# Performance work log

Measured on AMD Instinct MI355X. Metric: run time of the kernel, lower is better.

Reference implementation:

```python
import jax, jax.numpy as jnp
import numpy as np

N = 50000
E = 300000
D_IN = 128
H = 256
D_OUT = 256


def _glorot(key, shape):
    fan_in, fan_out = shape[0], shape[1]
    lim = float(np.sqrt(6.0 / (fan_in + fan_out)))
    return jax.random.uniform(key, shape, jnp.float32, -lim, lim)


def setup_inputs() -> dict:
    key = jax.random.key(0)
    ks = jax.random.split(key, 12)
    x = jax.random.normal(ks[0], (N, D_IN), jnp.float32)
    edge_index = jax.random.randint(ks[1], (2, E), 0, N, jnp.int64)
    return {
        "x": x,
        "edge_index": edge_index,
        "W1": _glorot(ks[2], (D_IN, H)),  "b1": jnp.zeros((H,), jnp.float32),
        "Wg1": _glorot(ks[3], (H, H)),    "bg1": jnp.zeros((H,), jnp.float32),
        "Wg2": _glorot(ks[4], (H, H)),    "bg2": jnp.zeros((H,), jnp.float32),
        "W2": _glorot(ks[5], (H, H)),     "b2": jnp.zeros((H,), jnp.float32),
        "W3": _glorot(ks[6], (H, D_OUT)), "b3": jnp.zeros((D_OUT,), jnp.float32),
    }


def _gcn_conv(h, src, dst, W, b):
    # PyG GCNConv: h' = D^-1/2 (A + I) D^-1/2 (h W) + b, deg counted at target with self-loops
    h = h @ W                                           # [N, H]
    deg = jnp.zeros((N,), h.dtype).at[dst].add(1.0) + 1.0
    dinv = jax.lax.rsqrt(deg)                           # deg^-1/2, [N]
    norm = dinv[src] * dinv[dst]                        # [E]
    msg = h[src] * norm[:, None]                        # gather + scale, [E, H]
    agg = jax.ops.segment_sum(msg, dst, num_segments=N)  # scatter-add
    agg = agg + h * (dinv * dinv)[:, None]              # self-loop contribution (norm = 1/deg)
    return agg + b


def reference(x, edge_index, W1, b1, Wg1, bg1, Wg2, bg2, W2, b2, W3, b3):
    src, dst = edge_index[0], edge_index[1]
    h = jax.nn.relu(x @ W1 + b1)
    h = jax.nn.relu(_gcn_conv(h, src, dst, Wg1, bg1))
    h = jax.nn.relu(_gcn_conv(h, src, dst, Wg2, bg2))
    h = jax.nn.relu(h @ W2 + b2)
    return jax.nn.softmax(h @ W3 + b3, axis=1)
```

## Files before the change

kernel.cpp:

```cpp
#include <hip/hip_runtime.h>
#include <math.h>

#define HDIM 256

typedef float floatx4 __attribute__((ext_vector_type(4)));
typedef __bf16 bf16x8 __attribute__((ext_vector_type(8)));
typedef unsigned short ushortx4 __attribute__((ext_vector_type(4)));
typedef unsigned short ushortx8 __attribute__((ext_vector_type(8)));

#define AS1C(p) ((const __attribute__((address_space(1))) void*)(p))
#define AS3(p)  ((__attribute__((address_space(3))) void*)(p))

__device__ inline unsigned short bf16_rn(float f) {
  unsigned u = __float_as_uint(f);
  return (unsigned short)((u + 0x7FFFu + ((u >> 16) & 1u)) >> 16);
}

__device__ inline void split_f32(float f, unsigned short& h, unsigned short& l) {
  unsigned short hb = bf16_rn(f);
  float hf = __uint_as_float(((unsigned)hb) << 16);
  h = hb;
  l = bf16_rn(f - hf);
}


__global__ __launch_bounds__(256)
void prep_w_staged(const float* __restrict__ W, unsigned short* __restrict__ SH,
                   unsigned short* __restrict__ SL, int K) {
  int idx = blockIdx.x * 256 + threadIdx.x;
  int total = K * 32;
  if (idx >= total) return;
  int chunksPerCb = total >> 1;
  int cb = (idx >= chunksPerCb) ? 1 : 0;
  int rem = idx - cb * chunksPerCb;
  int kt = rem >> 9;
  int chunk = rem & 511;
  int kc = chunk >> 7;
  int col = chunk & 127;
  const float* src = W + (size_t)(kt * 32 + kc * 8) * HDIM + cb * 128 + col;
#pragma unroll
  for (int e = 0; e < 8; ++e) {
    unsigned short h, l;
    split_f32(src[(size_t)e * HDIM], h, l);
    SH[(size_t)idx * 8 + e] = h;
    SL[(size_t)idx * 8 + e] = l;
  }
}


__global__ __launch_bounds__(256)
void split_plane(const float* __restrict__ in, unsigned short* __restrict__ H,
                 unsigned short* __restrict__ L, int total8) {
  int i = blockIdx.x * 256 + threadIdx.x;
  if (i >= total8) return;
  const float4* p = (const float4*)in;
  float4 v0 = p[(size_t)i * 2];
  float4 v1 = p[(size_t)i * 2 + 1];
  float f[8] = {v0.x, v0.y, v0.z, v0.w, v1.x, v1.y, v1.z, v1.w};
  ushortx8 hh, ll;
#pragma unroll
  for (int e = 0; e < 8; ++e) {
    unsigned short h, l;
    split_f32(f[e], h, l);
    hh[e] = h;
    ll[e] = l;
  }
  ((ushortx8*)H)[i] = hh;
  ((ushortx8*)L)[i] = ll;
}


__global__ __launch_bounds__(256)
void deg_count_kernel(const int* __restrict__ ei, int* __restrict__ deg, int E) {
  int e = blockIdx.x * 256 + threadIdx.x;
  if (e < E) atomicAdd(&deg[ei[E + e]], 1);
}

__global__ __launch_bounds__(256)
void dinv_kernel(const int* __restrict__ deg, float* __restrict__ dinv, int n) {
  int i = blockIdx.x * 256 + threadIdx.x;
  if (i < n) dinv[i] = 1.0f / sqrtf((float)deg[i] + 1.0f);
}

__global__ __launch_bounds__(256)
void block_sum_kernel(const int* __restrict__ deg, int* __restrict__ bsum, int n) {
  __shared__ int sm[256];
  int t = threadIdx.x;
  int idx = blockIdx.x * 256 + t;
  sm[t] = (idx < n) ? deg[idx] : 0;
  __syncthreads();
  for (int off = 128; off > 0; off >>= 1) {
    if (t < off) sm[t] += sm[t + off];
    __syncthreads();
  }
  if (t == 0) bsum[blockIdx.x] = sm[0];
}

__global__ __launch_bounds__(256)
void scan_bsums_kernel(const int* __restrict__ bsum, int* __restrict__ boff,
                       int* __restrict__ rowptr, int nb, int n) {
  __shared__ int sm[256];
  int t = threadIdx.x;
  int v = (t < nb) ? bsum[t] : 0;
  sm[t] = v;
  __syncthreads();
  for (int off = 1; off < 256; off <<= 1) {
    int a = (t >= off) ? sm[t - off] : 0;
    __syncthreads();
    sm[t] += a;
    __syncthreads();
  }
  if (t < nb) boff[t] = sm[t] - v;
  if (t == 255) rowptr[n] = sm[255];
}

__global__ __launch_bounds__(256)
void scan_final_kernel(const int* __restrict__ deg, const int* __restrict__ boff,
                       int* __restrict__ rowptr, int* __restrict__ cursor, int n) {
  __shared__ int sm[256];
  int t = threadIdx.x;
  int idx = blockIdx.x * 256 + t;
  int v = (idx < n) ? deg[idx] : 0;
  sm[t] = v;
  __syncthreads();
  for (int off = 1; off < 256; off <<= 1) {
    int a = (t >= off) ? sm[t - off] : 0;
    __syncthreads();
    sm[t] += a;
    __syncthreads();
  }
  int excl = sm[t] - v + boff[blockIdx.x];
  if (idx < n) { rowptr[idx] = excl; cursor[idx] = excl; }
}

__global__ __launch_bounds__(256)
void fill_csr_kernel(const int* __restrict__ ei, const float* __restrict__ dinv,
                     int* __restrict__ cursor, int* __restrict__ col,
                     float* __restrict__ wsrc, int E) {
  int e = blockIdx.x * 256 + threadIdx.x;
  if (e < E) {
    int s = ei[e];
    int d = ei[E + e];
    int p = atomicAdd(&cursor[d], 1);
    col[p] = s;
    wsrc[p] = dinv[s];
  }
}


template<bool BIAS, bool RELU, bool SPLIT_OUT>
__global__ __launch_bounds__(512, 4)
void mfma_gemm_p(const unsigned short* __restrict__ AH, const unsigned short* __restrict__ AL,
                 const unsigned short* __restrict__ SWH, const unsigned short* __restrict__ SWL,
                 const float* __restrict__ bias,
                 float* __restrict__ C, unsigned short* __restrict__ CH,
                 unsigned short* __restrict__ CL, int M, int K) {
  __shared__ __align__(16) unsigned short AsH[4096];
  __shared__ __align__(16) unsigned short AsL[4096];
  __shared__ __align__(16) unsigned short BsH[8192];
  __shared__ __align__(16) unsigned short BsL[8192];

  const int tid = threadIdx.x;
  const int w = tid >> 6;
  const int l = tid & 63;
  const int l15 = l & 15;
  const int quad = l >> 4;
  const int wm = w & 1;
  const int wn = w >> 1;
  const int bm = blockIdx.x * 128;
  const int ktc = K >> 5;
  const int chunksPerCb = ktc * 512;

  floatx4 acc[4][4];
#pragma unroll
  for (int i = 0; i < 4; ++i)
#pragma unroll
    for (int j = 0; j < 4; ++j) acc[i][j] = (floatx4){0.f, 0.f, 0.f, 0.f};

  for (int kt = 0; kt < ktc; ++kt) {
    __syncthreads();

    {
      int L = tid;
      int row = L >> 2;
      int p = L & 3;
      int kc = p ^ (row & 3) ^ ((row >> 2) & 3);
      int grow = bm + row;
      if (grow > M - 1) grow = M - 1;
      const unsigned short* gH = AH + (size_t)grow * K + kt * 32 + kc * 8;
      const unsigned short* gL = AL + (size_t)grow * K + kt * 32 + kc * 8;
      __builtin_amdgcn_global_load_lds(AS1C(gH), AS3(&AsH[(w * 64) * 8]), 16, 0, 0);
      __builtin_amdgcn_global_load_lds(AS1C(gL), AS3(&AsL[(w * 64) * 8]), 16, 0, 0);
    }
#pragma unroll
    for (int j = 0; j < 2; ++j) {
      int pos = j * 512 + w * 64 + l;
      int kc = pos >> 8;
      int within = pos & 255;
      int cb = within >> 7;
      int colL = within & 127;
      size_t gi = (size_t)cb * chunksPerCb + (size_t)kt * 512 + kc * 128 + colL;
      __builtin_amdgcn_global_load_lds(AS1C(SWH + gi * 8),
                                       AS3(&BsH[(j * 512 + w * 64) * 8]), 16, 0, 0);
      __builtin_amdgcn_global_load_lds(AS1C(SWL + gi * 8),
                                       AS3(&BsL[(j * 512 + w * 64) * 8]), 16, 0, 0);
    }

    __syncthreads();

    bf16x8 aH[4], aL[4];
#pragma unroll
    for (int fi = 0; fi < 4; ++fi) {
      int r = wm * 64 + fi * 16 + l15;
      int sw = quad ^ (r & 3) ^ ((r >> 2) & 3);
      aH[fi] = *(const bf16x8*)&AsH[(r * 4 + sw) * 8];
      aL[fi] = *(const bf16x8*)&AsL[(r * 4 + sw) * 8];
    }
#pragma unroll
    for (int fj = 0; fj < 4; ++fj) {
      int colG = wn * 64 + fj * 16 + l15;
      int cidx = quad * 256 + colG;
      bf16x8 bh = *(const bf16x8*)&BsH[cidx * 8];
      bf16x8 bl = *(const bf16x8*)&BsL[cidx * 8];
#pragma unroll
      for (int fi = 0; fi < 4; ++fi) {
        floatx4 t = acc[fi][fj];
        t = __builtin_amdgcn_mfma_f32_16x16x32_bf16(aH[fi], bl, t, 0, 0, 0);
        t = __builtin_amdgcn_mfma_f32_16x16x32_bf16(aL[fi], bh, t, 0, 0, 0);
        t = __builtin_amdgcn_mfma_f32_16x16x32_bf16(aH[fi], bh, t, 0, 0, 0);
        acc[fi][fj] = t;
      }
    }
  }

  float bcol[4];
#pragma unroll
  for (int fj = 0; fj < 4; ++fj)
    bcol[fj] = BIAS ? bias[wn * 64 + fj * 16 + l15] : 0.f;

#pragma unroll
  for (int fi = 0; fi < 4; ++fi) {
    int rb = bm + wm * 64 + fi * 16 + quad * 4;
#pragma unroll
    for (int r = 0; r < 4; ++r) {
      int row = rb + r;
      if (row < M) {
        size_t base = (size_t)row * HDIM + wn * 64 + l15;
        if (SPLIT_OUT) {
#pragma unroll
          for (int fj = 0; fj < 4; ++fj) {
            float v = acc[fi][fj][r] + bcol[fj];
            if (RELU) v = fmaxf(v, 0.f);
            unsigned short h, lo;
            split_f32(v, h, lo);
            CH[base + fj * 16] = h;
            CL[base + fj * 16] = lo;
          }
        } else {
#pragma unroll
          for (int fj = 0; fj < 4; ++fj) {
            float v = acc[fi][fj][r] + bcol[fj];
            if (RELU) v = fmaxf(v, 0.f);
            C[base + fj * 16] = v;
          }
        }
      }
    }
  }
}


__global__ __launch_bounds__(512, 4)
void mfma_gemm_softmax(const unsigned short* __restrict__ AH, const unsigned short* __restrict__ AL,
                       const unsigned short* __restrict__ SWH, const unsigned short* __restrict__ SWL,
                       const float* __restrict__ bias, float* __restrict__ out, int M, int K) {
  __shared__ __align__(16) unsigned short AsH[4096];
  __shared__ __align__(16) unsigned short AsL[4096];
  __shared__ __align__(16) unsigned short BsH[8192];
  __shared__ __align__(16) unsigned short BsL[8192];
  __shared__ float smax[128 * 4];
  __shared__ float ssum[128 * 4];

  const int tid = threadIdx.x;
  const int w = tid >> 6;
  const int l = tid & 63;
  const int l15 = l & 15;
  const int quad = l >> 4;
  const int wm = w & 1;
  const int wn = w >> 1;
  const int bm = blockIdx.x * 128;
  const int ktc = K >> 5;
  const int chunksPerCb = ktc * 512;

  floatx4 acc[4][4];
#pragma unroll
  for (int i = 0; i < 4; ++i)
#pragma unroll
    for (int j = 0; j < 4; ++j) acc[i][j] = (floatx4){0.f, 0.f, 0.f, 0.f};

  for (int kt = 0; kt < ktc; ++kt) {
    __syncthreads();

    {
      int L = tid;
      int row = L >> 2;
      int p = L & 3;
      int kc = p ^ (row & 3) ^ ((row >> 2) & 3);
      int grow = bm + row;
      if (grow > M - 1) grow = M - 1;
      const unsigned short* gH = AH + (size_t)grow * K + kt * 32 + kc * 8;
      const unsigned short* gL = AL + (size_t)grow * K + kt * 32 + kc * 8;
      __builtin_amdgcn_global_load_lds(AS1C(gH), AS3(&AsH[(w * 64) * 8]), 16, 0, 0);
      __builtin_amdgcn_global_load_lds(AS1C(gL), AS3(&AsL[(w * 64) * 8]), 16, 0, 0);
    }
#pragma unroll
    for (int j = 0; j < 2; ++j) {
      int pos = j * 512 + w * 64 + l;
      int kc = pos >> 8;
      int within = pos & 255;
      int cb = within >> 7;
      int colL = within & 127;
      size_t gi = (size_t)cb * chunksPerCb + (size_t)kt * 512 + kc * 128 + colL;
      __builtin_amdgcn_global_load_lds(AS1C(SWH + gi * 8),
                                       AS3(&BsH[(j * 512 + w * 64) * 8]), 16, 0, 0);
      __builtin_amdgcn_global_load_lds(AS1C(SWL + gi * 8),
                                       AS3(&BsL[(j * 512 + w * 64) * 8]), 16, 0, 0);
    }

    __syncthreads();

    bf16x8 aH[4], aL[4];
#pragma unroll
    for (int fi = 0; fi < 4; ++fi) {
      int r = wm * 64 + fi * 16 + l15;
      int sw = quad ^ (r & 3) ^ ((r >> 2) & 3);
      aH[fi] = *(const bf16x8*)&AsH[(r * 4 + sw) * 8];
      aL[fi] = *(const bf16x8*)&AsL[(r * 4 + sw) * 8];
    }
#pragma unroll
    for (int fj = 0; fj < 4; ++fj) {
      int colG = wn * 64 + fj * 16 + l15;
      int cidx = quad * 256 + colG;
      bf16x8 bh = *(const bf16x8*)&BsH[cidx * 8];
      bf16x8 bl = *(const bf16x8*)&BsL[cidx * 8];
#pragma unroll
      for (int fi = 0; fi < 4; ++fi) {
        floatx4 t = acc[fi][fj];
        t = __builtin_amdgcn_mfma_f32_16x16x32_bf16(aH[fi], bl, t, 0, 0, 0);
        t = __builtin_amdgcn_mfma_f32_16x16x32_bf16(aL[fi], bh, t, 0, 0, 0);
        t = __builtin_amdgcn_mfma_f32_16x16x32_bf16(aH[fi], bh, t, 0, 0, 0);
        acc[fi][fj] = t;
      }
    }
  }

  float bcol[4];
#pragma unroll
  for (int fj = 0; fj < 4; ++fj)
    bcol[fj] = bias[wn * 64 + fj * 16 + l15];

#pragma unroll
  for (int fi = 0; fi < 4; ++fi) {
#pragma unroll
    for (int r = 0; r < 4; ++r) {
      float mv = -3.4e38f;
#pragma unroll
      for (int fj = 0; fj < 4; ++fj) mv = fmaxf(mv, acc[fi][fj][r] + bcol[fj]);
#pragma unroll
      for (int off = 1; off < 16; off <<= 1) mv = fmaxf(mv, __shfl_xor(mv, off));
      int row = wm * 64 + fi * 16 + quad * 4 + r;
      if (l15 == 0) smax[row * 4 + wn] = mv;
    }
  }
  __syncthreads();

#pragma unroll
  for (int fi = 0; fi < 4; ++fi) {
#pragma unroll
    for (int r = 0; r < 4; ++r) {
      int row = wm * 64 + fi * 16 + quad * 4 + r;
      float gm = fmaxf(fmaxf(smax[row * 4 + 0], smax[row * 4 + 1]),
                       fmaxf(smax[row * 4 + 2], smax[row * 4 + 3]));
      float s = 0.f;
#pragma unroll
      for (int fj = 0; fj < 4; ++fj) {
        float p = expf(acc[fi][fj][r] + bcol[fj] - gm);
        acc[fi][fj][r] = p;
        s += p;
      }
#pragma unroll
      for (int off = 1; off < 16; off <<= 1) s += __shfl_xor(s, off);
      if (l15 == 0) ssum[row * 4 + wn] = s;
    }
  }
  __syncthreads();

#pragma unroll
  for (int fi = 0; fi < 4; ++fi) {
#pragma unroll
    for (int r = 0; r < 4; ++r) {
      int row = wm * 64 + fi * 16 + quad * 4 + r;
      int grow = bm + row;
      if (grow < M) {
        float inv = 1.0f / (ssum[row * 4 + 0] + ssum[row * 4 + 1] +
                            ssum[row * 4 + 2] + ssum[row * 4 + 3]);
        float* Cp = out + (size_t)grow * HDIM + wn * 64 + l15;
#pragma unroll
        for (int fj = 0; fj < 4; ++fj) Cp[fj * 16] = acc[fi][fj][r] * inv;
      }
    }
  }
}


__global__ __launch_bounds__(256)
void aggregate_b(const float* __restrict__ t, const float* __restrict__ dinv,
                 const int* __restrict__ rowptr, const int* __restrict__ col,
                 const float* __restrict__ wsrc, const float* __restrict__ bias,
                 unsigned short* __restrict__ OH, unsigned short* __restrict__ OL, int n) {
  int gw = (int)((blockIdx.x * 256 + threadIdx.x) >> 6);
  int lane = threadIdx.x & 63;
  if (gw >= n) return;
  float di = dinv[gw];
  float4 v = ((const float4*)(t + (size_t)gw * HDIM))[lane];
  float ss = di * di;
  float a0 = v.x * ss, a1 = v.y * ss, a2 = v.z * ss, a3 = v.w * ss;
  int e0 = rowptr[gw], e1 = rowptr[gw + 1];

  for (int base = e0; base < e1; base += 8) {
    int cs[8];
    float wv[8];
#pragma unroll
    for (int i = 0; i < 8; ++i) {
      int e = base + i;
      if (e > e1 - 1) e = e1 - 1;
      cs[i] = col[e];
      wv[i] = wsrc[e];
    }
    float wg[8];
#pragma unroll
    for (int i = 0; i < 8; ++i)
      wg[i] = (base + i < e1) ? wv[i] * di : 0.f;
    float4 rw[8];
#pragma unroll
    for (int i = 0; i < 8; ++i)
      rw[i] = ((const float4*)(t + (size_t)cs[i] * HDIM))[lane];
#pragma unroll
    for (int i = 0; i < 8; ++i) {
      a0 = fmaf(rw[i].x, wg[i], a0);
      a1 = fmaf(rw[i].y, wg[i], a1);
      a2 = fmaf(rw[i].z, wg[i], a2);
      a3 = fmaf(rw[i].w, wg[i], a3);
    }
  }

  float4 bb = ((const float4*)bias)[lane];
  float r0 = fmaxf(a0 + bb.x, 0.f);
  float r1 = fmaxf(a1 + bb.y, 0.f);
  float r2 = fmaxf(a2 + bb.z, 0.f);
  float r3 = fmaxf(a3 + bb.w, 0.f);
  unsigned short h0, h1, h2, h3, l0, l1, l2, l3;
  split_f32(r0, h0, l0);
  split_f32(r1, h1, l1);
  split_f32(r2, h2, l2);
  split_f32(r3, h3, l3);
  ((ushortx4*)(OH + (size_t)gw * HDIM))[lane] = (ushortx4){h0, h1, h2, h3};
  ((ushortx4*)(OL + (size_t)gw * HDIM))[lane] = (ushortx4){l0, l1, l2, l3};
}


extern "C" void kernel_launch(void* const* d_in, const int* in_sizes, int n_in,
                              void* d_out, int out_size, void* d_ws, size_t ws_size,
                              hipStream_t stream) {
  const float* x   = (const float*)d_in[0];
  const int*   ei  = (const int*)d_in[1];
  const float* W1  = (const float*)d_in[2];
  const float* b1  = (const float*)d_in[3];
  const float* Wg1 = (const float*)d_in[4];
  const float* bg1 = (const float*)d_in[5];
  const float* Wg2 = (const float*)d_in[6];
  const float* bg2 = (const float*)d_in[7];
  const float* W2  = (const float*)d_in[8];
  const float* b2  = (const float*)d_in[9];
  const float* W3  = (const float*)d_in[10];
  const float* b3  = (const float*)d_in[11];
  float* out = (float*)d_out;

  const int K1 = in_sizes[2] / HDIM;
  const int N  = in_sizes[0] / K1;
  const int E  = in_sizes[1] / 2;

  char* w = (char*)d_ws;
  auto alloc = [&](size_t bytes) -> char* {
    char* p = w;
    w += (bytes + 255) & ~(size_t)255;
    return p;
  };
  unsigned short* PH = (unsigned short*)alloc((size_t)N * HDIM * 2);
  unsigned short* PL = (unsigned short*)alloc((size_t)N * HDIM * 2);
  float* dinv   = (float*)alloc((size_t)N * sizeof(float));
  int*   deg    = (int*)alloc((size_t)N * sizeof(int));
  int*   rowptr = (int*)alloc((size_t)(N + 1) * sizeof(int));
  int*   cursor = (int*)alloc((size_t)N * sizeof(int));
  int*   col    = (int*)alloc((size_t)E * sizeof(int));
  float* wcsr   = (float*)alloc((size_t)E * sizeof(float));
  const int nb  = (N + 255) / 256;
  int*   bsum   = (int*)alloc((size_t)nb * sizeof(int));
  int*   boff   = (int*)alloc((size_t)nb * sizeof(int));
  unsigned short* W1sH  = (unsigned short*)alloc((size_t)HDIM * K1 * 2);
  unsigned short* W1sL  = (unsigned short*)alloc((size_t)HDIM * K1 * 2);
  unsigned short* Wg1sH = (unsigned short*)alloc((size_t)HDIM * HDIM * 2);
  unsigned short* Wg1sL = (unsigned short*)alloc((size_t)HDIM * HDIM * 2);
  unsigned short* Wg2sH = (unsigned short*)alloc((size_t)HDIM * HDIM * 2);
  unsigned short* Wg2sL = (unsigned short*)alloc((size_t)HDIM * HDIM * 2);
  unsigned short* W2sH  = (unsigned short*)alloc((size_t)HDIM * HDIM * 2);
  unsigned short* W2sL  = (unsigned short*)alloc((size_t)HDIM * HDIM * 2);
  unsigned short* W3sH  = (unsigned short*)alloc((size_t)HDIM * HDIM * 2);
  unsigned short* W3sL  = (unsigned short*)alloc((size_t)HDIM * HDIM * 2);

  unsigned short* XH = (unsigned short*)out;
  unsigned short* XL = XH + (size_t)N * K1;
  unsigned short* QH = (unsigned short*)out;
  unsigned short* QL = QH + (size_t)N * HDIM;

  const int ge = (E + 255) / 256;
  const int gn = (N + 255) / 256;

  prep_w_staged<<<(K1 * 32 + 255) / 256, 256, 0, stream>>>(W1, W1sH, W1sL, K1);
  prep_w_staged<<<(HDIM * 32 + 255) / 256, 256, 0, stream>>>(Wg1, Wg1sH, Wg1sL, HDIM);
  prep_w_staged<<<(HDIM * 32 + 255) / 256, 256, 0, stream>>>(Wg2, Wg2sH, Wg2sL, HDIM);
  prep_w_staged<<<(HDIM * 32 + 255) / 256, 256, 0, stream>>>(W2, W2sH, W2sL, HDIM);
  prep_w_staged<<<(HDIM * 32 + 255) / 256, 256, 0, stream>>>(W3, W3sH, W3sL, HDIM);

  hipMemsetAsync(deg, 0, (size_t)N * sizeof(int), stream);
  deg_count_kernel<<<ge, 256, 0, stream>>>(ei, deg, E);
  dinv_kernel<<<gn, 256, 0, stream>>>(deg, dinv, N);
  block_sum_kernel<<<nb, 256, 0, stream>>>(deg, bsum, N);
  scan_bsums_kernel<<<1, 256, 0, stream>>>(bsum, boff, rowptr, nb, N);
  scan_final_kernel<<<nb, 256, 0, stream>>>(deg, boff, rowptr, cursor, N);
  fill_csr_kernel<<<ge, 256, 0, stream>>>(ei, dinv, cursor, col, wcsr, E);

  const int g128 = (N + 127) / 128;
  const int gagg = (N + 3) / 4;
  const int tot8 = N * K1 / 8;

  split_plane<<<(tot8 + 255) / 256, 256, 0, stream>>>(x, XH, XL, tot8);
  mfma_gemm_p<true, true, true><<<g128, 512, 0, stream>>>(XH, XL, W1sH, W1sL, b1, nullptr, PH, PL, N, K1);
  mfma_gemm_p<false, false, false><<<g128, 512, 0, stream>>>(PH, PL, Wg1sH, Wg1sL, nullptr, out, nullptr, nullptr, N, HDIM);
  aggregate_b<<<gagg, 256, 0, stream>>>(out, dinv, rowptr, col, wcsr, bg1, PH, PL, N);
  mfma_gemm_p<false, false, false><<<g128, 512, 0, stream>>>(PH, PL, Wg2sH, Wg2sL, nullptr, out, nullptr, nullptr, N, HDIM);
  aggregate_b<<<gagg, 256, 0, stream>>>(out, dinv, rowptr, col, wcsr, bg2, PH, PL, N);
  mfma_gemm_p<true, true, true><<<g128, 512, 0, stream>>>(PH, PL, W2sH, W2sL, b2, nullptr, QH, QL, N, HDIM);
  mfma_gemm_softmax<<<g128, 512, 0, stream>>>(QH, QL, W3sH, W3sL, b3, out, N, HDIM);
}
```

Baseline: 403.8 us.

## Fuse weight prep, dinv, and input split; make aggregation grid-stride

Measured after the change: 395.2 us. 2.1% less time.

```diff
diff --git a/kernel.cpp b/kernel.cpp
--- a/kernel.cpp
+++ b/kernel.cpp
@@ -24,12 +24,10 @@
 }
 
 
-__global__ __launch_bounds__(256)
-void prep_w_staged(const float* __restrict__ W, unsigned short* __restrict__ SH,
-                   unsigned short* __restrict__ SL, int K) {
-  int idx = blockIdx.x * 256 + threadIdx.x;
+__device__ inline void prep_w_body(const float* __restrict__ W,
+                                   unsigned short* __restrict__ SH,
+                                   unsigned short* __restrict__ SL, int K, int idx) {
   int total = K * 32;
-  if (idx >= total) return;
   int chunksPerCb = total >> 1;
   int cb = (idx >= chunksPerCb) ? 1 : 0;
   int rem = idx - cb * chunksPerCb;
@@ -47,26 +45,31 @@
   }
 }
 
-
 __global__ __launch_bounds__(256)
-void split_plane(const float* __restrict__ in, unsigned short* __restrict__ H,
-                 unsigned short* __restrict__ L, int total8) {
-  int i = blockIdx.x * 256 + threadIdx.x;
-  if (i >= total8) return;
-  const float4* p = (const float4*)in;
-  float4 v0 = p[(size_t)i * 2];
-  float4 v1 = p[(size_t)i * 2 + 1];
-  float f[8] = {v0.x, v0.y, v0.z, v0.w, v1.x, v1.y, v1.z, v1.w};
-  ushortx8 hh, ll;
-#pragma unroll
-  for (int e = 0; e < 8; ++e) {
-    unsigned short h, l;
-    split_f32(f[e], h, l);
-    hh[e] = h;
-    ll[e] = l;
-  }
-  ((ushortx8*)H)[i] = hh;
-  ((ushortx8*)L)[i] = ll;
+void prep_w_all(const float* __restrict__ W1, unsigned short* __restrict__ S1H,
+                unsigned short* __restrict__ S1L, int K1,
+                const float* __restrict__ Wg1, unsigned short* __restrict__ G1H,
+                unsigned short* __restrict__ G1L,
+                const float* __restrict__ Wg2, unsigned short* __restrict__ G2H,
+                unsigned short* __restrict__ G2L,
+                const float* __restrict__ W2, unsigned short* __restrict__ S2H,
+                unsigned short* __restrict__ S2L,
+                const float* __restrict__ W3, unsigned short* __restrict__ S3H,
+                unsigned short* __restrict__ S3L) {
+  int gidx = blockIdx.x * 256 + threadIdx.x;
+  int t1 = K1 * 32;
+  int t256 = HDIM * 32;
+  if (gidx < t1) {
+    prep_w_body(W1, S1H, S1L, K1, gidx);
+    return;
+  }
+  int r = gidx - t1;
+  int which = r / t256;
+  int idx = r - which * t256;
+  if (which == 0)      prep_w_body(Wg1, G1H, G1L, HDIM, idx);
+  else if (which == 1) prep_w_body(Wg2, G2H, G2L, HDIM, idx);
+  else if (which == 2) prep_w_body(W2, S2H, S2L, HDIM, idx);
+  else if (which == 3) prep_w_body(W3, S3H, S3L, HDIM, idx);
 }
 
 
@@ -77,17 +80,14 @@
 }
 
 __global__ __launch_bounds__(256)
-void dinv_kernel(const int* __restrict__ deg, float* __restrict__ dinv, int n) {
-  int i = blockIdx.x * 256 + threadIdx.x;
-  if (i < n) dinv[i] = 1.0f / sqrtf((float)deg[i] + 1.0f);
-}
-
-__global__ __launch_bounds__(256)
-void block_sum_kernel(const int* __restrict__ deg, int* __restrict__ bsum, int n) {
+void block_sum_kernel(const int* __restrict__ deg, int* __restrict__ bsum,
+                      float* __restrict__ dinv, int n) {
   __shared__ int sm[256];
   int t = threadIdx.x;
   int idx = blockIdx.x * 256 + t;
-  sm[t] = (idx < n) ? deg[idx] : 0;
+  int v = (idx < n) ? deg[idx] : 0;
+  sm[t] = v;
+  if (idx < n) dinv[idx] = 1.0f / sqrtf((float)v + 1.0f);
   __syncthreads();
   for (int off = 128; off > 0; off >>= 1) {
     if (t < off) sm[t] += sm[t + off];
@@ -148,6 +148,131 @@
 }
 
 
+template<bool BIAS, bool RELU>
+__global__ __launch_bounds__(512, 4)
+void mfma_gemm_sA(const float* __restrict__ A,
+                  const unsigned short* __restrict__ SWH, const unsigned short* __restrict__ SWL,
+                  const float* __restrict__ bias,
+                  unsigned short* __restrict__ CH, unsigned short* __restrict__ CL,
+                  int M, int K) {
+  __shared__ __align__(16) unsigned short AsH[4096];
+  __shared__ __align__(16) unsigned short AsL[4096];
+  __shared__ __align__(16) unsigned short BsH[8192];
+  __shared__ __align__(16) unsigned short BsL[8192];
+
+  const int tid = threadIdx.x;
+  const int w = tid >> 6;
+  const int l = tid & 63;
+  const int l15 = l & 15;
+  const int quad = l >> 4;
+  const int wm = w & 1;
+  const int wn = w >> 1;
+  const int bm = blockIdx.x * 128;
+  const int ktc = K >> 5;
+  const int chunksPerCb = ktc * 512;
+
+  floatx4 acc[4][4];
+#pragma unroll
+  for (int i = 0; i < 4; ++i)
+#pragma unroll
+    for (int j = 0; j < 4; ++j) acc[i][j] = (floatx4){0.f, 0.f, 0.f, 0.f};
+
+  const int arow = tid >> 2;
+  const int ap = tid & 3;
+  const int akc = ap ^ (arow & 3) ^ ((arow >> 2) & 3);
+  int agrow = bm + arow;
+  if (agrow > M - 1) agrow = M - 1;
+  const float* agp = A + (size_t)agrow * K + akc * 8;
+
+  for (int kt = 0; kt < ktc; ++kt) {
+    float4 f0 = *(const float4*)(agp + kt * 32);
+    float4 f1 = *(const float4*)(agp + kt * 32 + 4);
+
+    __syncthreads();
+
+#pragma unroll
+    for (int j = 0; j < 2; ++j) {
+      int pos = j * 512 + w * 64 + l;
+      int kc = pos >> 8;
+      int within = pos & 255;
+      int cb = within >> 7;
+      int colL = within & 127;
+      size_t gi = (size_t)cb * chunksPerCb + (size_t)kt * 512 + kc * 128 + colL;
+      __builtin_amdgcn_global_load_lds(AS1C(SWH + gi * 8),
+                                       AS3(&BsH[(j * 512 + w * 64) * 8]), 16, 0, 0);
+      __builtin_amdgcn_global_load_lds(AS1C(SWL + gi * 8),
+                                       AS3(&BsL[(j * 512 + w * 64) * 8]), 16, 0, 0);
+    }
+
+    {
+      float f[8] = {f0.x, f0.y, f0.z, f0.w, f1.x, f1.y, f1.z, f1.w};
+      ushortx8 hh, ll;
+#pragma unroll
+      for (int e = 0; e < 8; ++e) {
+        unsigned short h, lo;
+        split_f32(f[e], h, lo);
+        hh[e] = h;
+        ll[e] = lo;
+      }
+      *(ushortx8*)&AsH[(size_t)tid * 8] = hh;
+      *(ushortx8*)&AsL[(size_t)tid * 8] = ll;
+    }
+
+    __syncthreads();
+
+    bf16x8 aH[4], aL[4];
+#pragma unroll
+    for (int fi = 0; fi < 4; ++fi) {
+      int r = wm * 64 + fi * 16 + l15;
+      int sw = quad ^ (r & 3) ^ ((r >> 2) & 3);
+      aH[fi] = *(const bf16x8*)&AsH[(r * 4 + sw) * 8];
+      aL[fi] = *(const bf16x8*)&AsL[(r * 4 + sw) * 8];
+    }
+#pragma unroll
+    for (int fj = 0; fj < 4; ++fj) {
+      int colG = wn * 64 + fj * 16 + l15;
+      int cidx = quad * 256 + colG;
+      bf16x8 bh = *(const bf16x8*)&BsH[cidx * 8];
+      bf16x8 bl = *(const bf16x8*)&BsL[cidx * 8];
+#pragma unroll
+      for (int fi = 0; fi < 4; ++fi) {
+        floatx4 t = acc[fi][fj];
+        t = __builtin_amdgcn_mfma_f32_16x16x32_bf16(aH[fi], bl, t, 0, 0, 0);
+        t = __builtin_amdgcn_mfma_f32_16x16x32_bf16(aL[fi], bh, t, 0, 0, 0);
+        t = __builtin_amdgcn_mfma_f32_16x16x32_bf16(aH[fi], bh, t, 0, 0, 0);
+        acc[fi][fj] = t;
+      }
+    }
+  }
+
+  float bcol[4];
+#pragma unroll
+  for (int fj = 0; fj < 4; ++fj)
+    bcol[fj] = BIAS ? bias[wn * 64 + fj * 16 + l15] : 0.f;
+
+#pragma unroll
+  for (int fi = 0; fi < 4; ++fi) {
+    int rb = bm + wm * 64 + fi * 16 + quad * 4;
+#pragma unroll
+    for (int r = 0; r < 4; ++r) {
+      int row = rb + r;
+      if (row < M) {
+        size_t base = (size_t)row * HDIM + wn * 64 + l15;
+#pragma unroll
+        for (int fj = 0; fj < 4; ++fj) {
+          float v = acc[fi][fj][r] + bcol[fj];
+          if (RELU) v = fmaxf(v, 0.f);
+          unsigned short h, lo;
+          split_f32(v, h, lo);
+          CH[base + fj * 16] = h;
+          CL[base + fj * 16] = lo;
+        }
+      }
+    }
+  }
+}
+
+
 template<bool BIAS, bool RELU, bool SPLIT_OUT>
 __global__ __launch_bounds__(512, 4)
 void mfma_gemm_p(const unsigned short* __restrict__ AH, const unsigned short* __restrict__ AL,
@@ -418,54 +543,57 @@
                  const int* __restrict__ rowptr, const int* __restrict__ col,
                  const float* __restrict__ wsrc, const float* __restrict__ bias,
                  unsigned short* __restrict__ OH, unsigned short* __restrict__ OL, int n) {
-  int gw = (int)((blockIdx.x * 256 + threadIdx.x) >> 6);
-  int lane = threadIdx.x & 63;
-  if (gw >= n) return;
-  float di = dinv[gw];
-  float4 v = ((const float4*)(t + (size_t)gw * HDIM))[lane];
-  float ss = di * di;
-  float a0 = v.x * ss, a1 = v.y * ss, a2 = v.z * ss, a3 = v.w * ss;
-  int e0 = rowptr[gw], e1 = rowptr[gw + 1];
-
-  for (int base = e0; base < e1; base += 8) {
-    int cs[8];
-    float wv[8];
-#pragma unroll
-    for (int i = 0; i < 8; ++i) {
-      int e = base + i;
-      if (e > e1 - 1) e = e1 - 1;
-      cs[i] = col[e];
-      wv[i] = wsrc[e];
-    }
-    float wg[8];
-#pragma unroll
-    for (int i = 0; i < 8; ++i)
-      wg[i] = (base + i < e1) ? wv[i] * di : 0.f;
-    float4 rw[8];
-#pragma unroll
-    for (int i = 0; i < 8; ++i)
-      rw[i] = ((const float4*)(t + (size_t)cs[i] * HDIM))[lane];
-#pragma unroll
-    for (int i = 0; i < 8; ++i) {
-      a0 = fmaf(rw[i].x, wg[i], a0);
-      a1 = fmaf(rw[i].y, wg[i], a1);
-      a2 = fmaf(rw[i].z, wg[i], a2);
-      a3 = fmaf(rw[i].w, wg[i], a3);
-    }
-  }
-
+  const int nwave = (int)(gridDim.x << 2);
+  const int wid0 = (int)((blockIdx.x * 256 + threadIdx.x) >> 6);
+  const int lane = threadIdx.x & 63;
   float4 bb = ((const float4*)bias)[lane];
-  float r0 = fmaxf(a0 + bb.x, 0.f);
-  float r1 = fmaxf(a1 + bb.y, 0.f);
-  float r2 = fmaxf(a2 + bb.z, 0.f);
-  float r3 = fmaxf(a3 + bb.w, 0.f);
-  unsigned short h0, h1, h2, h3, l0, l1, l2, l3;
-  split_f32(r0, h0, l0);
-  split_f32(r1, h1, l1);
-  split_f32(r2, h2, l2);
-  split_f32(r3, h3, l3);
-  ((ushortx4*)(OH + (size_t)gw * HDIM))[lane] = (ushortx4){h0, h1, h2, h3};
-  ((ushortx4*)(OL + (size_t)gw * HDIM))[lane] = (ushortx4){l0, l1, l2, l3};
+
+  for (int gw = wid0; gw < n; gw += nwave) {
+    float di = dinv[gw];
+    float4 v = ((const float4*)(t + (size_t)gw * HDIM))[lane];
+    float ss = di * di;
+    float a0 = v.x * ss, a1 = v.y * ss, a2 = v.z * ss, a3 = v.w * ss;
+    int e0 = rowptr[gw], e1 = rowptr[gw + 1];
+
+    for (int base = e0; base < e1; base += 8) {
+      int cs[8];
+      float wv[8];
+#pragma unroll
+      for (int i = 0; i < 8; ++i) {
+        int e = base + i;
+        if (e > e1 - 1) e = e1 - 1;
+        cs[i] = col[e];
+        wv[i] = wsrc[e];
+      }
+      float wg[8];
+#pragma unroll
+      for (int i = 0; i < 8; ++i)
+        wg[i] = (base + i < e1) ? wv[i] * di : 0.f;
+      float4 rw[8];
+#pragma unroll
+      for (int i = 0; i < 8; ++i)
+        rw[i] = ((const float4*)(t + (size_t)cs[i] * HDIM))[lane];
+#pragma unroll
+      for (int i = 0; i < 8; ++i) {
+        a0 = fmaf(rw[i].x, wg[i], a0);
+        a1 = fmaf(rw[i].y, wg[i], a1);
+        a2 = fmaf(rw[i].z, wg[i], a2);
+        a3 = fmaf(rw[i].w, wg[i], a3);
+      }
+    }
+
+    float r0 = fmaxf(a0 + bb.x, 0.f);
+    float r1 = fmaxf(a1 + bb.y, 0.f);
+    float r2 = fmaxf(a2 + bb.z, 0.f);
+    float r3 = fmaxf(a3 + bb.w, 0.f);
+    unsigned short h0, h1, h2, h3, l0, l1, l2, l3;
+    split_f32(r0, h0, l0);
+    split_f32(r1, h1, l1);
+    split_f32(r2, h2, l2);
+    split_f32(r3, h3, l3);
+    ((ushortx4*)(OH + (size_t)gw * HDIM))[lane] = (ushortx4){h0, h1, h2, h3};
+    ((ushortx4*)(OL + (size_t)gw * HDIM))[lane] = (ushortx4){l0, l1, l2, l3};
+  }
 }
 
 
@@ -518,34 +646,27 @@
   unsigned short* W3sH  = (unsigned short*)alloc((size_t)HDIM * HDIM * 2);
   unsigned short* W3sL  = (unsigned short*)alloc((size_t)HDIM * HDIM * 2);
 
-  unsigned short* XH = (unsigned short*)out;
-  unsigned short* XL = XH + (size_t)N * K1;
   unsigned short* QH = (unsigned short*)out;
   unsigned short* QL = QH + (size_t)N * HDIM;
 
   const int ge = (E + 255) / 256;
-  const int gn = (N + 255) / 256;
-
-  prep_w_staged<<<(K1 * 32 + 255) / 256, 256, 0, stream>>>(W1, W1sH, W1sL, K1);
-  prep_w_staged<<<(HDIM * 32 + 255) / 256, 256, 0, stream>>>(Wg1, Wg1sH, Wg1sL, HDIM);
-  prep_w_staged<<<(HDIM * 32 + 255) / 256, 256, 0, stream>>>(Wg2, Wg2sH, Wg2sL, HDIM);
-  prep_w_staged<<<(HDIM * 32 + 255) / 256, 256, 0, stream>>>(W2, W2sH, W2sL, HDIM);
-  prep_w_staged<<<(HDIM * 32 + 255) / 256, 256, 0, stream>>>(W3, W3sH, W3sL, HDIM);
+
+  const int prepChunks = K1 * 32 + 4 * HDIM * 32;
+  prep_w_all<<<(prepChunks + 255) / 256, 256, 0, stream>>>(
+      W1, W1sH, W1sL, K1, Wg1, Wg1sH, Wg1sL, Wg2, Wg2sH, Wg2sL,
+      W2, W2sH, W2sL, W3, W3sH, W3sL);
 
   hipMemsetAsync(deg, 0, (size_t)N * sizeof(int), stream);
   deg_count_kernel<<<ge, 256, 0, stream>>>(ei, deg, E);
-  dinv_kernel<<<gn, 256, 0, stream>>>(deg, dinv, N);
-  block_sum_kernel<<<nb, 256, 0, stream>>>(deg, bsum, N);
+  block_sum_kernel<<<nb, 256, 0, stream>>>(deg, bsum, dinv, N);
   scan_bsums_kernel<<<1, 256, 0, stream>>>(bsum, boff, rowptr, nb, N);
   scan_final_kernel<<<nb, 256, 0, stream>>>(deg, boff, rowptr, cursor, N);
   fill_csr_kernel<<<ge, 256, 0, stream>>>(ei, dinv, cursor, col, wcsr, E);
 
   const int g128 = (N + 127) / 128;
-  const int gagg = (N + 3) / 4;
-  const int tot8 = N * K1 / 8;
-
-  split_plane<<<(tot8 + 255) / 256, 256, 0, stream>>>(x, XH, XL, tot8);
-  mfma_gemm_p<true, true, true><<<g128, 512, 0, stream>>>(XH, XL, W1sH, W1sL, b1, nullptr, PH, PL, N, K1);
+  const int gagg = 2048;
+
+  mfma_gemm_sA<true, true><<<g128, 512, 0, stream>>>(x, W1sH, W1sL, b1, PH, PL, N, K1);
   mfma_gemm_p<false, false, false><<<g128, 512, 0, stream>>>(PH, PL, Wg1sH, Wg1sL, nullptr, out, nullptr, nullptr, N, HDIM);
   aggregate_b<<<gagg, 256, 0, stream>>>(out, dinv, rowptr, col, wcsr, bg1, PH, PL, N);
   mfma_gemm_p<false, false, false><<<g128, 512, 0, stream>>>(PH, PL, Wg2sH, Wg2sL, nullptr, out, nullptr, nullptr, N, HDIM);
```
